# Kernel optimization log

Measured on AMD Instinct MI355X. Metric: run time of the kernel, lower is better.

The kernel has to match this reference:

```python
import jax, jax.numpy as jnp
import numpy as np

BS, CIN, H, W = 1, 128, 448, 96
CLASSES = (8, 8, 8)
PAD = (0, 4, 4)
DIV = 1  # c3_line_div
K2 = H * CLASSES[0]                 # 3584 CondMul experts for stage 2
K3 = H * CLASSES[0] * CLASSES[1]    # 28672 CondMul experts for stage 3
C1_DIMS = [(128, 32), (32, 32), (32, 8)]
C2_DIMS = [(128, 32), (32, 32), (32, 16)]
C3_DIMS = [(128, 32), (32, 32), (32, 16)]


def _cond_mul(x, inds, w, b):
    # per-row expert gather then small matmul: [N,i] x [N,i,o] -> [N,o]
    return jnp.einsum('ni,nio->no', x, w[inds]) + b[inds]


def setup_inputs() -> dict:
    key = jax.random.key(0)
    ks = jax.random.split(key, 19)
    d = {'x_in': jax.random.normal(ks[0], (BS, CIN, H, W), jnp.float32)}
    k = 1
    for tag, dims, nexp in (('1', C1_DIMS, H), ('2', C2_DIMS, K2), ('3', C3_DIMS, K3)):
        for i, (ci, co) in enumerate(dims):
            if tag == '1':
                d['w1_%d' % i] = jax.random.normal(ks[k], (H, co, ci), jnp.float32) * 0.1
            else:
                d['w%s_%d' % (tag, i)] = jax.random.normal(ks[k], (nexp, ci, co), jnp.float32) * 0.1
            d['b%s_%d' % (tag, i)] = jax.random.normal(ks[k + 1], (nexp, co), jnp.float32) * 0.1
            k += 2
    return d


def reference(x_in, w1_0, b1_0, w1_1, b1_1, w1_2, b1_2,
              w2_0, b2_0, w2_1, b2_1, w2_2, b2_2,
              w3_0, b3_0, w3_1, b3_1, w3_2, b3_2):
    bs, cin, h, w = x_in.shape
    c12 = CLASSES[0] * CLASSES[1]
    c123 = c12 * CLASSES[2]
    lrelu = jax.nn.leaky_relu  # slope 0.01, matches F.leaky_relu default
    hoff = jnp.arange(h, dtype=jnp.int32)[None, :, None]  # [1,H,1] line offsets

    # stage 1: grouped 1x1 conv (one group per image line)
    x = jnp.transpose(x_in, (0, 2, 1, 3))  # [bs,H,C,W]
    x = lrelu(jnp.einsum('hoi,bhiw->bhow', w1_0, x) + b1_0[None, :, :, None])
    x = lrelu(jnp.einsum('hoi,bhiw->bhow', w1_1, x) + b1_1[None, :, :, None])
    x = jnp.einsum('hoi,bhiw->bhow', w1_2, x) + b1_2[None, :, :, None]  # [bs,H,cls1,W]
    inds1 = jnp.argmax(x, axis=2).astype(jnp.int32)  # [bs,H,W]
    inds1_l = (inds1 + CLASSES[0] * hoff).reshape(-1)  # [N]

    x_l = jnp.transpose(x_in, (0, 2, 3, 1)).reshape(-1, cin)  # [N,C], N=bs*H*W

    # stage 2: CondMul cascade routed by inds1
    x = lrelu(_cond_mul(x_l, inds1_l, w2_0, b2_0))
    x = lrelu(_cond_mul(x, inds1_l, w2_1, b2_1))
    x = _cond_mul(x, inds1_l, w2_2, b2_2)
    inds2 = jnp.argmax(x, axis=-1).astype(jnp.int32).reshape(bs, h, w)
    inds12 = inds1 * CLASSES[1] + (inds2 - PAD[1])
    inds12_cl = jnp.clip(inds12, 0, c12 - 1)
    inds12_l = (inds12_cl + c12 * hoff).reshape(-1)
    inds12_s = (inds12_cl + c12 * (hoff // DIV)).reshape(-1)

    # stage 3: CondMul cascade routed by inds12
    x = lrelu(_cond_mul(x_l, inds12_s, w3_0, b3_0))
    x = lrelu(_cond_mul(x, inds12_s, w3_1, b3_1))
    x3 = _cond_mul(x, inds12_l, w3_2, b3_2)  # [N, cls3+2*pad3]
    inds3 = jnp.argmax(x3, axis=-1).astype(jnp.int32).reshape(bs, h, w)

    inds123 = jnp.clip(inds12 * CLASSES[2] + (inds3 - PAD[2]), 0, c123 - 1)
    return inds123.reshape(bs, 1, h, w)
```

## Files before the change

kernel.cpp:

```cpp
#include <hip/hip_runtime.h>

#define H_ 448
#define W_ 96
#define CIN_ 128
#define HW_ (H_*W_)

__device__ __forceinline__ float lrelu(float v){ return v > 0.0f ? v : 0.01f*v; }

template<int NC>
__device__ __forceinline__ void sort_by_class(const unsigned char* s_cls, short* s_perm,
                                              int* s_cnt, int* s_off, int t)
{
    if (t < NC){
        int c = 0;
        for (int p = 0; p < 96; p++) if (s_cls[p] == (unsigned char)t) c++;
        s_cnt[t] = c;
    }
    __syncthreads();
    if (t == 0){
        int a = 0;
        for (int c = 0; c < NC; c++){ s_off[c] = a; a += s_cnt[c]; }
    }
    __syncthreads();
    if (t < NC){
        int o = s_off[t];
        for (int p = 0; p < 96; p++) if (s_cls[p] == (unsigned char)t) s_perm[o++] = (short)p;
    }
    __syncthreads();
}

__global__ __launch_bounds__(768, 6)
void cls3_fused(const float* __restrict__ X,
                const float* __restrict__ w1_0, const float* __restrict__ b1_0,
                const float* __restrict__ w1_1, const float* __restrict__ b1_1,
                const float* __restrict__ w1_2, const float* __restrict__ b1_2,
                const float* __restrict__ w2_0, const float* __restrict__ b2_0,
                const float* __restrict__ w2_1, const float* __restrict__ b2_1,
                const float* __restrict__ w2_2, const float* __restrict__ b2_2,
                const float* __restrict__ w3_0, const float* __restrict__ b3_0,
                const float* __restrict__ w3_1, const float* __restrict__ b3_1,
                const float* __restrict__ w3_2, const float* __restrict__ b3_2,
                int* __restrict__ out)
{
    __shared__ float s_w0[4096];
    __shared__ float s_w1[1024];
    __shared__ float s_w2[256];
    __shared__ float s_A[96*36];
    __shared__ float s_B[96*36];
    __shared__ unsigned char s_cls[96];
    __shared__ unsigned char s_cls2[96];
    __shared__ short s_perm[96];
    __shared__ int   s_raw[96];
    __shared__ int   s_cnt[64];
    __shared__ int   s_off[64];

    const int h  = blockIdx.x;
    const int t  = threadIdx.x;

    {
        const int w  = t % 96;
        const int s  = t / 96;
        const int hw = h*96 + w;

        if (t < 384){
            const float* g0 = w1_0 + (size_t)h*4096;
            for (int j = t; j < 4096; j += 384) s_w0[j] = g0[j];
            const float* g1 = w1_1 + (size_t)h*1024;
            for (int j = t; j < 1024; j += 384) s_w1[j] = g1[j];
            const float* g2 = w1_2 + (size_t)h*256;
            for (int j = t; j < 256; j += 384) s_w2[j] = g2[j];
        } else {
            const int tt = t - 384;
            float keep = 0.f;
            const float4* p0 = (const float4*)(w2_0 + (size_t)h*32768);
            for (int v = tt; v < 8192; v += 384){ const float4 q = p0[v]; keep += q.x+q.y+q.z+q.w; }
            const float4* p1 = (const float4*)(w2_1 + (size_t)h*8192);
            for (int v = tt; v < 2048; v += 384){ const float4 q = p1[v]; keep += q.x+q.y+q.z+q.w; }
            const float4* p2 = (const float4*)(w2_2 + (size_t)h*4096);
            for (int v = tt; v < 1024; v += 384){ const float4 q = p2[v]; keep += q.x+q.y+q.z+q.w; }
            asm volatile("" :: "v"(keep));
        }
        __syncthreads();

        if (t < 384){
            float acc[8];
            const float* bp = b1_0 + h*32 + s*8;
            #pragma unroll
            for (int k=0;k<8;k++) acc[k] = bp[k];
            #pragma unroll 4
            for (int i4=0;i4<32;i4++){
                const float x0 = X[(size_t)(4*i4+0)*HW_ + hw];
                const float x1 = X[(size_t)(4*i4+1)*HW_ + hw];
                const float x2 = X[(size_t)(4*i4+2)*HW_ + hw];
                const float x3 = X[(size_t)(4*i4+3)*HW_ + hw];
                #pragma unroll
                for (int k=0;k<8;k++){
                    const float4 q = *(const float4*)&s_w0[(s*8+k)*128 + 4*i4];
                    acc[k] += x0*q.x; acc[k] += x1*q.y; acc[k] += x2*q.z; acc[k] += x3*q.w;
                }
            }
            #pragma unroll
            for (int k=0;k<8;k++) s_A[w*33 + s*8 + k] = lrelu(acc[k]);
        }
        __syncthreads();

        if (t < 384){
            float acc[8];
            const float* bp = b1_1 + h*32 + s*8;
            #pragma unroll
            for (int k=0;k<8;k++) acc[k] = bp[k];
            #pragma unroll
            for (int i4=0;i4<8;i4++){
                const float x0 = s_A[w*33 + 4*i4+0];
                const float x1 = s_A[w*33 + 4*i4+1];
                const float x2 = s_A[w*33 + 4*i4+2];
                const float x3 = s_A[w*33 + 4*i4+3];
                #pragma unroll
                for (int k=0;k<8;k++){
                    const float4 q = *(const float4*)&s_w1[(s*8+k)*32 + 4*i4];
                    acc[k] += x0*q.x; acc[k] += x1*q.y; acc[k] += x2*q.z; acc[k] += x3*q.w;
                }
            }
            #pragma unroll
            for (int k=0;k<8;k++) s_B[w*33 + s*8 + k] = lrelu(acc[k]);
        }
        __syncthreads();

        if (t < 384){
            float acc[2];
            const float* bp = b1_2 + h*8 + s*2;
            acc[0] = bp[0]; acc[1] = bp[1];
            #pragma unroll
            for (int i4=0;i4<8;i4++){
                const float x0 = s_B[w*33 + 4*i4+0];
                const float x1 = s_B[w*33 + 4*i4+1];
                const float x2 = s_B[w*33 + 4*i4+2];
                const float x3 = s_B[w*33 + 4*i4+3];
                #pragma unroll
                for (int k=0;k<2;k++){
                    const float4 q = *(const float4*)&s_w2[(s*2+k)*32 + 4*i4];
                    acc[k] += x0*q.x; acc[k] += x1*q.y; acc[k] += x2*q.z; acc[k] += x3*q.w;
                }
            }
            s_A[w*33 + s*2 + 0] = acc[0];
            s_A[w*33 + s*2 + 1] = acc[1];
        }
        __syncthreads();

        if (t < 96){
            const float* sc = &s_A[t*33];
            float best = sc[0]; int bi = 0;
            #pragma unroll
            for (int k=1;k<8;k++){ const float v = sc[k]; if (v > best){ best = v; bi = k; } }
            s_cls[t] = (unsigned char)bi;
        }
        __syncthreads();
    }

    sort_by_class<8>(s_cls, s_perm, s_cnt, s_off, t);

    const int p = t >> 3;
    const int j = t & 7;
    {
        const int sp = s_perm[p];
        const int c  = s_cls[sp];
        const long e = (long)h*8 + c;
        const int hw = h*96 + sp;
        const float* W0 = w2_0 + e*4096 + j*4;
        const float* W1 = w2_1 + e*1024 + j*4;
        const float* W2 = w2_2 + e*512  + j*2;

        float4 acc = *(const float4*)&b2_0[e*32 + j*4];
        #pragma unroll 8
        for (int i=0;i<128;i++){
            const float xv = X[(size_t)i*HW_ + hw];
            const float4 q = *(const float4*)&W0[i*32];
            acc.x += xv*q.x; acc.y += xv*q.y; acc.z += xv*q.z; acc.w += xv*q.w;
        }
        *(float4*)&s_A[p*36 + j*4] = make_float4(lrelu(acc.x),lrelu(acc.y),lrelu(acc.z),lrelu(acc.w));
        __syncthreads();

        float4 ac2 = *(const float4*)&b2_1[e*32 + j*4];
        #pragma unroll 8
        for (int i=0;i<32;i++){
            const float xv = s_A[p*36 + i];
            const float4 q = *(const float4*)&W1[i*32];
            ac2.x += xv*q.x; ac2.y += xv*q.y; ac2.z += xv*q.z; ac2.w += xv*q.w;
        }
        *(float4*)&s_B[p*36 + j*4] = make_float4(lrelu(ac2.x),lrelu(ac2.y),lrelu(ac2.z),lrelu(ac2.w));
        __syncthreads();

        float2 sc = *(const float2*)&b2_2[e*16 + j*2];
        #pragma unroll 8
        for (int i=0;i<32;i++){
            const float xv = s_B[p*36 + i];
            const float2 r = *(const float2*)&W2[i*16];
            sc.x += xv*r.x; sc.y += xv*r.y;
        }
        float best = sc.x; int bi = j*2;
        if (sc.y > best){ best = sc.y; bi = j*2+1; }
        #pragma unroll
        for (int off=1; off<8; off<<=1){
            const float ob = __shfl_xor(best, off, 64);
            const int  obi = __shfl_xor(bi,  off, 64);
            if (ob > best || (ob == best && obi < bi)){ best = ob; bi = obi; }
        }
        __syncthreads();
        if (j == 0){
            const int raw = c*8 + bi - 4;
            s_raw[sp]  = raw;
            s_cls2[sp] = (unsigned char)(raw < 0 ? 0 : (raw > 63 ? 63 : raw));
        }
        __syncthreads();
    }

    sort_by_class<64>(s_cls2, s_perm, s_cnt, s_off, t);

    {
        float keep = 0.f;
        for (int c = 0; c < 64; c++){
            if (s_cnt[c] == 0) continue;
            const long e = (long)h*64 + c;
            const float4* p0 = (const float4*)(w3_0 + e*4096);
            for (int v = t; v < 1024; v += 768){ const float4 q = p0[v]; keep += q.x+q.y+q.z+q.w; }
            const float4* p1 = (const float4*)(w3_1 + e*1024);
            if (t < 256){ const float4 q = p1[t]; keep += q.x+q.y+q.z+q.w; }
            const float4* p2 = (const float4*)(w3_2 + e*512);
            if (t < 128){ const float4 q = p2[t]; keep += q.x+q.y+q.z+q.w; }
        }
        asm volatile("" :: "v"(keep));
    }

    {
        const int sp = s_perm[p];
        const int c  = s_cls2[sp];
        const long e = (long)h*64 + c;
        const int hw = h*96 + sp;
        const float* W0 = w3_0 + e*4096 + j*4;
        const float* W1 = w3_1 + e*1024 + j*4;
        const float* W2 = w3_2 + e*512  + j*2;

        float4 acc = *(const float4*)&b3_0[e*32 + j*4];
        #pragma unroll 8
        for (int i=0;i<128;i++){
            const float xv = X[(size_t)i*HW_ + hw];
            const float4 q = *(const float4*)&W0[i*32];
            acc.x += xv*q.x; acc.y += xv*q.y; acc.z += xv*q.z; acc.w += xv*q.w;
        }
        *(float4*)&s_A[p*36 + j*4] = make_float4(lrelu(acc.x),lrelu(acc.y),lrelu(acc.z),lrelu(acc.w));
        __syncthreads();

        float4 ac2 = *(const float4*)&b3_1[e*32 + j*4];
        #pragma unroll 8
        for (int i=0;i<32;i++){
            const float xv = s_A[p*36 + i];
            const float4 q = *(const float4*)&W1[i*32];
            ac2.x += xv*q.x; ac2.y += xv*q.y; ac2.z += xv*q.z; ac2.w += xv*q.w;
        }
        *(float4*)&s_B[p*36 + j*4] = make_float4(lrelu(ac2.x),lrelu(ac2.y),lrelu(ac2.z),lrelu(ac2.w));
        __syncthreads();

        float2 sc = *(const float2*)&b3_2[e*16 + j*2];
        #pragma unroll 8
        for (int i=0;i<32;i++){
            const float xv = s_B[p*36 + i];
            const float2 r = *(const float2*)&W2[i*16];
            sc.x += xv*r.x; sc.y += xv*r.y;
        }
        float best = sc.x; int bi = j*2;
        if (sc.y > best){ best = sc.y; bi = j*2+1; }
        #pragma unroll
        for (int off=1; off<8; off<<=1){
            const float ob = __shfl_xor(best, off, 64);
            const int  obi = __shfl_xor(bi,  off, 64);
            if (ob > best || (ob == best && obi < bi)){ best = ob; bi = obi; }
        }
        if (j == 0){
            int v = s_raw[sp]*8 + bi - 4;
            v = v < 0 ? 0 : (v > 511 ? 511 : v);
            out[h*96 + sp] = v;
        }
    }
}

extern "C" void kernel_launch(void* const* d_in, const int* in_sizes, int n_in,
                              void* d_out, int out_size, void* d_ws, size_t ws_size,
                              hipStream_t stream) {
    const float* X    = (const float*)d_in[0];
    const float* w1_0 = (const float*)d_in[1];
    const float* b1_0 = (const float*)d_in[2];
    const float* w1_1 = (const float*)d_in[3];
    const float* b1_1 = (const float*)d_in[4];
    const float* w1_2 = (const float*)d_in[5];
    const float* b1_2 = (const float*)d_in[6];
    const float* w2_0 = (const float*)d_in[7];
    const float* b2_0 = (const float*)d_in[8];
    const float* w2_1 = (const float*)d_in[9];
    const float* b2_1 = (const float*)d_in[10];
    const float* w2_2 = (const float*)d_in[11];
    const float* b2_2 = (const float*)d_in[12];
    const float* w3_0 = (const float*)d_in[13];
    const float* b3_0 = (const float*)d_in[14];
    const float* w3_1 = (const float*)d_in[15];
    const float* b3_1 = (const float*)d_in[16];
    const float* w3_2 = (const float*)d_in[17];
    const float* b3_2 = (const float*)d_in[18];
    int* out = (int*)d_out;

    cls3_fused<<<H_, 768, 0, stream>>>(X,
        w1_0, b1_0, w1_1, b1_1, w1_2, b1_2,
        w2_0, b2_0, w2_1, b2_1, w2_2, b2_2,
        w3_0, b3_0, w3_1, b3_1, w3_2, b3_2,
        out);
}
```

Before: 184.6 us.

## Batch same-expert pixels into 4-row chunks to reuse CondMul weight loads

Restructures the stage 2 and 3 CondMul cascades so each 16-lane group handles a chunk of up to 4 pixels sharing the same expert. Each weight load is then reused across 4 pixels instead of being fetched once per pixel. The block shrinks from 768 to 384 threads, and the warm-up prefetch loops that touched w2 and w3 weights are removed. In exchange, chunk construction runs serially on one thread, partially filled chunks leave lanes idle, and the argmax becomes a 16-lane shuffle reduction.

Result: slower. 327.0 us (+77.2%).

```diff
diff --git a/kernel.cpp b/kernel.cpp
--- a/kernel.cpp
+++ b/kernel.cpp
@@ -29,7 +29,22 @@
     __syncthreads();
 }
 
-__global__ __launch_bounds__(768, 6)
+template<int NC>
+__device__ __forceinline__ void build_chunks(const int* s_cnt, const int* s_off,
+                                             int* s_chunk, int* s_nch, int t)
+{
+    if (t == 0){
+        int n = 0;
+        for (int c = 0; c < NC; c++){
+            const int cnt = s_cnt[c];
+            for (int b = 0; b < cnt; b += 4) s_chunk[n++] = (c << 16) | (s_off[c] + b);
+        }
+        *s_nch = n;
+    }
+    __syncthreads();
+}
+
+__global__ __launch_bounds__(384, 4)
 void cls3_fused(const float* __restrict__ X,
                 const float* __restrict__ w1_0, const float* __restrict__ b1_0,
                 const float* __restrict__ w1_1, const float* __restrict__ b1_1,
@@ -53,6 +68,8 @@
     __shared__ int   s_raw[96];
     __shared__ int   s_cnt[64];
     __shared__ int   s_off[64];
+    __shared__ int   s_chunk[96];
+    __shared__ int   s_nch;
 
     const int h  = blockIdx.x;
     const int t  = threadIdx.x;
@@ -62,27 +79,15 @@
         const int s  = t / 96;
         const int hw = h*96 + w;
 
-        if (t < 384){
-            const float* g0 = w1_0 + (size_t)h*4096;
-            for (int j = t; j < 4096; j += 384) s_w0[j] = g0[j];
-            const float* g1 = w1_1 + (size_t)h*1024;
-            for (int j = t; j < 1024; j += 384) s_w1[j] = g1[j];
-            const float* g2 = w1_2 + (size_t)h*256;
-            for (int j = t; j < 256; j += 384) s_w2[j] = g2[j];
-        } else {
-            const int tt = t - 384;
-            float keep = 0.f;
-            const float4* p0 = (const float4*)(w2_0 + (size_t)h*32768);
-            for (int v = tt; v < 8192; v += 384){ const float4 q = p0[v]; keep += q.x+q.y+q.z+q.w; }
-            const float4* p1 = (const float4*)(w2_1 + (size_t)h*8192);
-            for (int v = tt; v < 2048; v += 384){ const float4 q = p1[v]; keep += q.x+q.y+q.z+q.w; }
-            const float4* p2 = (const float4*)(w2_2 + (size_t)h*4096);
-            for (int v = tt; v < 1024; v += 384){ const float4 q = p2[v]; keep += q.x+q.y+q.z+q.w; }
-            asm volatile("" :: "v"(keep));
-        }
-        __syncthreads();
-
-        if (t < 384){
+        const float* g0 = w1_0 + (size_t)h*4096;
+        for (int j = t; j < 4096; j += 384) s_w0[j] = g0[j];
+        const float* g1 = w1_1 + (size_t)h*1024;
+        for (int j = t; j < 1024; j += 384) s_w1[j] = g1[j];
+        const float* g2 = w1_2 + (size_t)h*256;
+        for (int j = t; j < 256; j += 384) s_w2[j] = g2[j];
+        __syncthreads();
+
+        {
             float acc[8];
             const float* bp = b1_0 + h*32 + s*8;
             #pragma unroll
@@ -104,7 +109,7 @@
         }
         __syncthreads();
 
-        if (t < 384){
+        {
             float acc[8];
             const float* bp = b1_1 + h*32 + s*8;
             #pragma unroll
@@ -126,7 +131,7 @@
         }
         __syncthreads();
 
-        if (t < 384){
+        {
             float acc[2];
             const float* bp = b1_2 + h*8 + s*2;
             acc[0] = bp[0]; acc[1] = bp[1];
@@ -157,128 +162,187 @@
         __syncthreads();
     }
 
+    const int g = t >> 4;
+    const int l = t & 15;
+
     sort_by_class<8>(s_cls, s_perm, s_cnt, s_off, t);
-
-    const int p = t >> 3;
-    const int j = t & 7;
+    build_chunks<8>(s_cnt, s_off, s_chunk, &s_nch, t);
     {
-        const int sp = s_perm[p];
-        const int c  = s_cls[sp];
-        const long e = (long)h*8 + c;
-        const int hw = h*96 + sp;
-        const float* W0 = w2_0 + e*4096 + j*4;
-        const float* W1 = w2_1 + e*1024 + j*4;
-        const float* W2 = w2_2 + e*512  + j*2;
-
-        float4 acc = *(const float4*)&b2_0[e*32 + j*4];
-        #pragma unroll 8
-        for (int i=0;i<128;i++){
-            const float xv = X[(size_t)i*HW_ + hw];
-            const float4 q = *(const float4*)&W0[i*32];
-            acc.x += xv*q.x; acc.y += xv*q.y; acc.z += xv*q.z; acc.w += xv*q.w;
-        }
-        *(float4*)&s_A[p*36 + j*4] = make_float4(lrelu(acc.x),lrelu(acc.y),lrelu(acc.z),lrelu(acc.w));
-        __syncthreads();
-
-        float4 ac2 = *(const float4*)&b2_1[e*32 + j*4];
-        #pragma unroll 8
-        for (int i=0;i<32;i++){
-            const float xv = s_A[p*36 + i];
-            const float4 q = *(const float4*)&W1[i*32];
-            ac2.x += xv*q.x; ac2.y += xv*q.y; ac2.z += xv*q.z; ac2.w += xv*q.w;
-        }
-        *(float4*)&s_B[p*36 + j*4] = make_float4(lrelu(ac2.x),lrelu(ac2.y),lrelu(ac2.z),lrelu(ac2.w));
-        __syncthreads();
-
-        float2 sc = *(const float2*)&b2_2[e*16 + j*2];
-        #pragma unroll 8
-        for (int i=0;i<32;i++){
-            const float xv = s_B[p*36 + i];
-            const float2 r = *(const float2*)&W2[i*16];
-            sc.x += xv*r.x; sc.y += xv*r.y;
-        }
-        float best = sc.x; int bi = j*2;
-        if (sc.y > best){ best = sc.y; bi = j*2+1; }
-        #pragma unroll
-        for (int off=1; off<8; off<<=1){
-            const float ob = __shfl_xor(best, off, 64);
-            const int  obi = __shfl_xor(bi,  off, 64);
-            if (ob > best || (ob == best && obi < bi)){ best = ob; bi = obi; }
-        }
-        __syncthreads();
-        if (j == 0){
-            const int raw = c*8 + bi - 4;
-            s_raw[sp]  = raw;
-            s_cls2[sp] = (unsigned char)(raw < 0 ? 0 : (raw > 63 ? 63 : raw));
-        }
-        __syncthreads();
-    }
+        const int nch = s_nch;
+        for (int ck = g; ck < nch; ck += 24){
+            const int info = s_chunk[ck];
+            const int c    = info >> 16;
+            const int base = info & 0xffff;
+            const int rend = s_off[c] + s_cnt[c];
+            int idx[4]; bool val[4];
+            #pragma unroll
+            for (int k=0;k<4;k++){
+                int s0 = base + k;
+                val[k] = s0 < rend;
+                if (!val[k]) s0 = rend - 1;
+                idx[k] = s_perm[s0];
+            }
+            const long e = (long)h*8 + c;
+            const float* Xb = X + h*96;
+
+            const float2 bv0 = *(const float2*)&b2_0[e*32 + 2*l];
+            float2 a0=bv0, a1=bv0, a2=bv0, a3=bv0;
+            const float* W0 = w2_0 + e*4096 + 2*l;
+            #pragma unroll 8
+            for (int i=0;i<128;i++){
+                const float2 wq = *(const float2*)&W0[i*32];
+                const float x0 = Xb[(size_t)i*HW_ + idx[0]];
+                const float x1 = Xb[(size_t)i*HW_ + idx[1]];
+                const float x2 = Xb[(size_t)i*HW_ + idx[2]];
+                const float x3 = Xb[(size_t)i*HW_ + idx[3]];
+                a0.x += x0*wq.x; a0.y += x0*wq.y;
+                a1.x += x1*wq.x; a1.y += x1*wq.y;
+                a2.x += x2*wq.x; a2.y += x2*wq.y;
+                a3.x += x3*wq.x; a3.y += x3*wq.y;
+            }
+            if (val[0]) *(float2*)&s_A[idx[0]*36 + 2*l] = make_float2(lrelu(a0.x), lrelu(a0.y));
+            if (val[1]) *(float2*)&s_A[idx[1]*36 + 2*l] = make_float2(lrelu(a1.x), lrelu(a1.y));
+            if (val[2]) *(float2*)&s_A[idx[2]*36 + 2*l] = make_float2(lrelu(a2.x), lrelu(a2.y));
+            if (val[3]) *(float2*)&s_A[idx[3]*36 + 2*l] = make_float2(lrelu(a3.x), lrelu(a3.y));
+
+            const float2 bv1 = *(const float2*)&b2_1[e*32 + 2*l];
+            float2 c0=bv1, c1=bv1, c2=bv1, c3=bv1;
+            const float* W1 = w2_1 + e*1024 + 2*l;
+            #pragma unroll 8
+            for (int i=0;i<32;i++){
+                const float2 wq = *(const float2*)&W1[i*32];
+                const float x0 = s_A[idx[0]*36 + i];
+                const float x1 = s_A[idx[1]*36 + i];
+                const float x2 = s_A[idx[2]*36 + i];
+                const float x3 = s_A[idx[3]*36 + i];
+                c0.x += x0*wq.x; c0.y += x0*wq.y;
+                c1.x += x1*wq.x; c1.y += x1*wq.y;
+                c2.x += x2*wq.x; c2.y += x2*wq.y;
+                c3.x += x3*wq.x; c3.y += x3*wq.y;
+            }
+            if (val[0]) *(float2*)&s_B[idx[0]*36 + 2*l] = make_float2(lrelu(c0.x), lrelu(c0.y));
+            if (val[1]) *(float2*)&s_B[idx[1]*36 + 2*l] = make_float2(lrelu(c1.x), lrelu(c1.y));
+            if (val[2]) *(float2*)&s_B[idx[2]*36 + 2*l] = make_float2(lrelu(c2.x), lrelu(c2.y));
+            if (val[3]) *(float2*)&s_B[idx[3]*36 + 2*l] = make_float2(lrelu(c3.x), lrelu(c3.y));
+
+            float d0, d1, d2, d3;
+            d0 = d1 = d2 = d3 = b2_2[e*16 + l];
+            const float* W2 = w2_2 + e*512 + l;
+            #pragma unroll 8
+            for (int i=0;i<32;i++){
+                const float wq = W2[i*16];
+                d0 += s_B[idx[0]*36 + i]*wq;
+                d1 += s_B[idx[1]*36 + i]*wq;
+                d2 += s_B[idx[2]*36 + i]*wq;
+                d3 += s_B[idx[3]*36 + i]*wq;
+            }
+            float dd[4] = { d0, d1, d2, d3 };
+            #pragma unroll
+            for (int k=0;k<4;k++){
+                float best = dd[k]; int bi = l;
+                #pragma unroll
+                for (int off=1; off<16; off<<=1){
+                    const float ob = __shfl_xor(best, off, 64);
+                    const int  obi = __shfl_xor(bi,  off, 64);
+                    if (ob > best || (ob == best && obi < bi)){ best = ob; bi = obi; }
+                }
+                if (l == 0 && val[k]){
+                    const int raw = c*8 + bi - 4;
+                    s_raw[idx[k]]  = raw;
+                    s_cls2[idx[k]] = (unsigned char)(raw < 0 ? 0 : (raw > 63 ? 63 : raw));
+                }
+            }
+        }
+    }
+    __syncthreads();
 
     sort_by_class<64>(s_cls2, s_perm, s_cnt, s_off, t);
-
+    build_chunks<64>(s_cnt, s_off, s_chunk, &s_nch, t);
     {
-        float keep = 0.f;
-        for (int c = 0; c < 64; c++){
-            if (s_cnt[c] == 0) continue;
+        const int nch = s_nch;
+        for (int ck = g; ck < nch; ck += 24){
+            const int info = s_chunk[ck];
+            const int c    = info >> 16;
+            const int base = info & 0xffff;
+            const int rend = s_off[c] + s_cnt[c];
+            int idx[4]; bool val[4];
+            #pragma unroll
+            for (int k=0;k<4;k++){
+                int s0 = base + k;
+                val[k] = s0 < rend;
+                if (!val[k]) s0 = rend - 1;
+                idx[k] = s_perm[s0];
+            }
             const long e = (long)h*64 + c;
-            const float4* p0 = (const float4*)(w3_0 + e*4096);
-            for (int v = t; v < 1024; v += 768){ const float4 q = p0[v]; keep += q.x+q.y+q.z+q.w; }
-            const float4* p1 = (const float4*)(w3_1 + e*1024);
-            if (t < 256){ const float4 q = p1[t]; keep += q.x+q.y+q.z+q.w; }
-            const float4* p2 = (const float4*)(w3_2 + e*512);
-            if (t < 128){ const float4 q = p2[t]; keep += q.x+q.y+q.z+q.w; }
-        }
-        asm volatile("" :: "v"(keep));
-    }
-
-    {
-        const int sp = s_perm[p];
-        const int c  = s_cls2[sp];
-        const long e = (long)h*64 + c;
-        const int hw = h*96 + sp;
-        const float* W0 = w3_0 + e*4096 + j*4;
-        const float* W1 = w3_1 + e*1024 + j*4;
-        const float* W2 = w3_2 + e*512  + j*2;
-
-        float4 acc = *(const float4*)&b3_0[e*32 + j*4];
-        #pragma unroll 8
-        for (int i=0;i<128;i++){
-            const float xv = X[(size_t)i*HW_ + hw];
-            const float4 q = *(const float4*)&W0[i*32];
-            acc.x += xv*q.x; acc.y += xv*q.y; acc.z += xv*q.z; acc.w += xv*q.w;
-        }
-        *(float4*)&s_A[p*36 + j*4] = make_float4(lrelu(acc.x),lrelu(acc.y),lrelu(acc.z),lrelu(acc.w));
-        __syncthreads();
-
-        float4 ac2 = *(const float4*)&b3_1[e*32 + j*4];
-        #pragma unroll 8
-        for (int i=0;i<32;i++){
-            const float xv = s_A[p*36 + i];
-            const float4 q = *(const float4*)&W1[i*32];
-            ac2.x += xv*q.x; ac2.y += xv*q.y; ac2.z += xv*q.z; ac2.w += xv*q.w;
-        }
-        *(float4*)&s_B[p*36 + j*4] = make_float4(lrelu(ac2.x),lrelu(ac2.y),lrelu(ac2.z),lrelu(ac2.w));
-        __syncthreads();
-
-        float2 sc = *(const float2*)&b3_2[e*16 + j*2];
-        #pragma unroll 8
-        for (int i=0;i<32;i++){
-            const float xv = s_B[p*36 + i];
-            const float2 r = *(const float2*)&W2[i*16];
-            sc.x += xv*r.x; sc.y += xv*r.y;
-        }
-        float best = sc.x; int bi = j*2;
-        if (sc.y > best){ best = sc.y; bi = j*2+1; }
-        #pragma unroll
-        for (int off=1; off<8; off<<=1){
-            const float ob = __shfl_xor(best, off, 64);
-            const int  obi = __shfl_xor(bi,  off, 64);
-            if (ob > best || (ob == best && obi < bi)){ best = ob; bi = obi; }
-        }
-        if (j == 0){
-            int v = s_raw[sp]*8 + bi - 4;
-            v = v < 0 ? 0 : (v > 511 ? 511 : v);
-            out[h*96 + sp] = v;
+            const float* Xb = X + h*96;
+
+            const float2 bv0 = *(const float2*)&b3_0[e*32 + 2*l];
+            float2 a0=bv0, a1=bv0, a2=bv0, a3=bv0;
+            const float* W0 = w3_0 + e*4096 + 2*l;
+            #pragma unroll 8
+            for (int i=0;i<128;i++){
+                const float2 wq = *(const float2*)&W0[i*32];
+                const float x0 = Xb[(size_t)i*HW_ + idx[0]];
+                const float x1 = Xb[(size_t)i*HW_ + idx[1]];
+                const float x2 = Xb[(size_t)i*HW_ + idx[2]];
+                const float x3 = Xb[(size_t)i*HW_ + idx[3]];
+                a0.x += x0*wq.x; a0.y += x0*wq.y;
+                a1.x += x1*wq.x; a1.y += x1*wq.y;
+                a2.x += x2*wq.x; a2.y += x2*wq.y;
+                a3.x += x3*wq.x; a3.y += x3*wq.y;
+            }
+            if (val[0]) *(float2*)&s_A[idx[0]*36 + 2*l] = make_float2(lrelu(a0.x), lrelu(a0.y));
+            if (val[1]) *(float2*)&s_A[idx[1]*36 + 2*l] = make_float2(lrelu(a1.x), lrelu(a1.y));
+            if (val[2]) *(float2*)&s_A[idx[2]*36 + 2*l] = make_float2(lrelu(a2.x), lrelu(a2.y));
+            if (val[3]) *(float2*)&s_A[idx[3]*36 + 2*l] = make_float2(lrelu(a3.x), lrelu(a3.y));
+
+            const float2 bv1 = *(const float2*)&b3_1[e*32 + 2*l];
+            float2 c0=bv1, c1=bv1, c2=bv1, c3=bv1;
+            const float* W1 = w3_1 + e*1024 + 2*l;
+            #pragma unroll 8
+            for (int i=0;i<32;i++){
+                const float2 wq = *(const float2*)&W1[i*32];
+                const float x0 = s_A[idx[0]*36 + i];
+                const float x1 = s_A[idx[1]*36 + i];
+                const float x2 = s_A[idx[2]*36 + i];
+                const float x3 = s_A[idx[3]*36 + i];
+                c0.x += x0*wq.x; c0.y += x0*wq.y;
+                c1.x += x1*wq.x; c1.y += x1*wq.y;
+                c2.x += x2*wq.x; c2.y += x2*wq.y;
+                c3.x += x3*wq.x; c3.y += x3*wq.y;
+            }
+            if (val[0]) *(float2*)&s_B[idx[0]*36 + 2*l] = make_float2(lrelu(c0.x), lrelu(c0.y));
+            if (val[1]) *(float2*)&s_B[idx[1]*36 + 2*l] = make_float2(lrelu(c1.x), lrelu(c1.y));
+            if (val[2]) *(float2*)&s_B[idx[2]*36 + 2*l] = make_float2(lrelu(c2.x), lrelu(c2.y));
+            if (val[3]) *(float2*)&s_B[idx[3]*36 + 2*l] = make_float2(lrelu(c3.x), lrelu(c3.y));
+
+            float d0, d1, d2, d3;
+            d0 = d1 = d2 = d3 = b3_2[e*16 + l];
+            const float* W2 = w3_2 + e*512 + l;
+            #pragma unroll 8
+            for (int i=0;i<32;i++){
+                const float wq = W2[i*16];
+                d0 += s_B[idx[0]*36 + i]*wq;
+                d1 += s_B[idx[1]*36 + i]*wq;
+                d2 += s_B[idx[2]*36 + i]*wq;
+                d3 += s_B[idx[3]*36 + i]*wq;
+            }
+            float dd[4] = { d0, d1, d2, d3 };
+            #pragma unroll
+            for (int k=0;k<4;k++){
+                float best = dd[k]; int bi = l;
+                #pragma unroll
+                for (int off=1; off<16; off<<=1){
+                    const float ob = __shfl_xor(best, off, 64);
+                    const int  obi = __shfl_xor(bi,  off, 64);
+                    if (ob > best || (ob == best && obi < bi)){ best = ob; bi = obi; }
+                }
+                if (l == 0 && val[k]){
+                    int v = s_raw[idx[k]]*8 + bi - 4;
+                    v = v < 0 ? 0 : (v > 511 ? 511 : v);
+                    out[h*96 + idx[k]] = v;
+                }
+            }
         }
     }
 }
@@ -307,7 +371,7 @@
     const float* b3_2 = (const float*)d_in[18];
     int* out = (int*)d_out;
 
-    cls3_fused<<<H_, 768, 0, stream>>>(X,
+    cls3_fused<<<H_, 384, 0, stream>>>(X,
         w1_0, b1_0, w1_1, b1_1, w1_2, b1_2,
         w2_0, b2_0, w2_1, b2_1, w2_2, b2_2,
         w3_0, b3_0, w3_1, b3_1, w3_2, b3_2,
```
